# Kernel tuning notes

Measured on AMD Instinct MI355X. Metric: run time of the kernel, lower is better.

## Reference

```python
import jax, jax.numpy as jnp
import numpy as np

L_COORD = 5.0
L_NOOBJ = 0.5
NUM_CLS = 20


def setup_inputs() -> dict:
    key = jax.random.key(0)
    k1, k2, k3, k4, k5, k6, k7 = jax.random.split(key, 7)
    BS, S, MAXOBJ = 2048, 14, 20
    # post-sigmoid style predictions in [0,1): [conf,x,y,w,h]*2 + 20 classes
    pred = jax.random.uniform(k1, (BS, S, S, 30), jnp.float32)
    # valid GT boxes: x1,y1,x2,y2 in [0,1] with positive w,h; class index stored as float
    x1 = jax.random.uniform(k2, (BS, MAXOBJ)) * 0.75
    y1 = jax.random.uniform(k3, (BS, MAXOBJ)) * 0.75
    w = jax.random.uniform(k4, (BS, MAXOBJ)) * 0.2 + 0.02
    h = jax.random.uniform(k5, (BS, MAXOBJ)) * 0.2 + 0.02
    cls = jax.random.randint(k6, (BS, MAXOBJ), 0, NUM_CLS).astype(jnp.float32)
    target = jnp.stack([x1, y1, x1 + w, y1 + h, cls], axis=-1)
    valid = (jax.random.uniform(k7, (BS, MAXOBJ)) > 0.3).astype(jnp.float32)
    target = target * valid[..., None]
    return {"pred": pred, "target": target}


def build_target(target, pred_boxes, grids):
    """target: (BS,MaxObj,5); pred_boxes: (BS,2,S,S,5) [conf,x,y,w,h].
    Returns confxywh (BS,2,S,S,5) and class one-hots (BS,S,S,20).
    Sequential scan over object slots preserves the torch loop's
    last-write-wins semantics when two objects land in the same cell."""
    bs = target.shape[0]
    bidx = jnp.arange(bs)
    conf0 = jnp.zeros((bs, 2, grids, grids, 5), pred_boxes.dtype)
    clc0 = jnp.zeros((bs, grids, grids, NUM_CLS), pred_boxes.dtype)
    fg = float(grids)

    def step(carry, obj):  # obj: (BS,5)
        conf, clc = carry
        x1, y1, x2, y2, cls = (obj[:, i] for i in range(5))
        valid = obj.sum(axis=1) != 0
        cx = (x1 + x2) * 0.5 * fg
        cy = (y1 + y2) * 0.5 * fg
        w = x2 - x1
        h = y2 - y1
        gx = jnp.clip(jnp.floor(cx).astype(jnp.int32), 0, grids - 1)
        gy = jnp.clip(jnp.floor(cy).astype(jnp.int32), 0, grids - 1)
        offx = cx - gx
        offy = cy - gy
        # responsible-cell predictions: (BS,2,5) -> xywh
        pb = pred_boxes[bidx, :, gy, gx]
        pxy = pb[..., 1:3] / fg
        pwh = pb[..., 3:5]
        p_lt = pxy - 0.5 * pwh
        p_rb = pxy + 0.5 * pwh
        t_ctr = jnp.stack([offx, offy], -1) / fg  # matches original (uses offsets, not cx/cy)
        t_wh = jnp.stack([w, h], -1)
        t_lt = t_ctr - 0.5 * t_wh
        t_rb = t_ctr + 0.5 * t_wh
        lt = jnp.maximum(p_lt, t_lt[:, None, :])
        rb = jnp.minimum(p_rb, t_rb[:, None, :])
        whi = jnp.clip(rb - lt, 0.0, None)
        inter = whi[..., 0] * whi[..., 1]
        a1 = (p_rb[..., 0] - p_lt[..., 0]) * (p_rb[..., 1] - p_lt[..., 1])
        a2 = ((t_rb[..., 0] - t_lt[..., 0]) * (t_rb[..., 1] - t_lt[..., 1]))[:, None]
        iou = inter / (a1 + a2 - inter)  # (BS,2)
        mi = jnp.argmax(iou, axis=1).astype(jnp.int32)
        # invalid rows: redirect to an out-of-range grid row, dropped by scatter
        gy_s = jnp.where(valid, gy, grids)
        vals = jnp.stack([jnp.ones_like(offx), offx, offy, w, h], -1)
        conf = conf.at[bidx, mi, gy_s, gx].set(vals, mode="drop")
        clc = clc.at[bidx, gy_s, gx, cls.astype(jnp.int32)].set(1.0, mode="drop")
        return (conf, clc), None

    (conf, clc), _ = jax.lax.scan(step, (conf0, clc0), jnp.swapaxes(target, 0, 1))
    return conf, clc


def _yolo_loss(pred, target):
    bs, S = pred.shape[0], pred.shape[2]
    pred_b = pred[..., :10].reshape(bs, S, S, 2, 5).transpose(0, 3, 1, 2, 4)  # (BS,2,S,S,5)
    pred_cls = pred[..., 10:]  # (BS,S,S,20)
    conf, clc = build_target(target, pred_b, S)

    conf_sum = conf[:, 0, :, :, 0] + conf[:, 1, :, :, 0]  # (BS,S,S)
    obj_m = conf_sum == 1.0
    noobj_m = conf_sum == 0.0
    noobj_m2 = jnp.broadcast_to(noobj_m[:, None], (bs, 2, S, S))

    n_noobj = jnp.sum(noobj_m2.astype(pred.dtype))
    noobj_loss = jnp.sum(noobj_m2 * (pred_b[..., 0] - conf[..., 0]) ** 2) / n_noobj

    # responsible box rows = obj cells AND non-zero target row (selectMask in torch)
    resp = obj_m[:, None] & (jnp.sum(conf, axis=-1) != 0)  # (BS,2,S,S)
    resp_f = resp.astype(pred.dtype)
    n_resp = jnp.sum(resp_f)

    objconf_loss = jnp.sum(resp_f * (pred_b[..., 0] - conf[..., 0]) ** 2) / n_resp
    loss_xy = jnp.sum(resp_f[..., None] * (pred_b[..., 1:3] - conf[..., 1:3]) ** 2) / (n_resp * 2.0)

    # safe sqrt: masked-out entries replaced by 1.0 to keep grads finite
    rm = resp[..., None]
    p_wh = jnp.sqrt(jnp.where(rm, pred_b[..., 3:5], 1.0))
    t_wh = jnp.sqrt(jnp.where(rm, conf[..., 3:5], 1.0))
    loss_wh = jnp.sum(resp_f[..., None] * (p_wh - t_wh) ** 2) / (n_resp * 2.0)

    obj_f = obj_m.astype(pred.dtype)
    n_obj = jnp.sum(obj_f)
    loss_clc = jnp.sum(obj_f[..., None] * (pred_cls - clc) ** 2) / (n_obj * NUM_CLS)

    return L_COORD * (loss_xy + loss_wh) + objconf_loss + L_NOOBJ * noobj_loss + loss_clc


def reference(pred, target):
    return _yolo_loss(pred, target)
```

## Files before the change

### kernel.cpp

```cpp
#include <hip/hip_runtime.h>
#include <math.h>

#define NBATCH 2048
#define GS 14
#define NCELL (GS * GS)
#define NCH 30
#define NPRED (NCELL * NCH)
#define MAXOBJ 20
#define NCLS 20
#define THREADS 256
#define BLOCKS 512

#define NWIN 200704
#define NWORK (NWIN * 4)
#define TOT_THREADS (BLOCKS * THREADS)
#define NITER 7

typedef float v4f __attribute__((ext_vector_type(4)));


__global__ __launch_bounds__(256) void yolo_main_kernel(
        const float* __restrict__ pred,
        const float* __restrict__ target,
        float* __restrict__ ws)
{
    __shared__ float s_red[4][8];
    const int blk = blockIdx.x;
    const int tid = threadIdx.x;
    const int wave = tid >> 6;
    const int lane = tid & 63;
    const float fg = (float)GS;
    const int b = blk * 4 + wave;
    const int gtid = blk * THREADS + tid;

    v4f xr[NITER];
    int wm_[NITER];
    {
        const v4f* g4 = (const v4f*)pred;
        #pragma unroll
        for (int k = 0; k < NITER; ++k) {
            int w = gtid + k * TOT_THREADS;
            int wc = (w < NWORK) ? w : (NWORK - 1);
            int g = wc >> 2;
            int m = wc & 3;
            int q = g * 15 + (m & 1) + ((m >> 1) * 7);
            wm_[k] = (w < NWORK) ? m : -1;
            xr[k] = __builtin_nontemporal_load(&g4[q]);
        }
    }

    float t0 = 0.f, t1 = 0.f, t2 = 0.f, t3 = 0.f, t4 = 0.f;
    if (lane < MAXOBJ) {
        const float* tb = target + (size_t)b * (MAXOBJ * 5) + lane * 5;
        t0 = tb[0]; t1 = tb[1]; t2 = tb[2]; t3 = tb[3]; t4 = tb[4];
    }

    float acc = 0.f;
    #pragma unroll
    for (int k = 0; k < NITER; ++k) {
        int m = wm_[k];
        if (m >= 0) {
            v4f x = xr[k];
            float val = (m == 0) ? x[0] : (m == 1) ? x[1] : (m == 2) ? x[2] : x[3];
            acc += val * val;
        }
    }

    float v0 = 0.f, v1 = 0.f, v2 = 0.f, v3 = 0.f, v4 = 0.f, v5 = 0.f, v6 = 0.f;
    {
        const int o = lane;
        bool valid = false;
        int cell = 0, mi = 0, cls = 0;
        float offx = 0.f, offy = 0.f, w = 0.f, h = 0.f;
        float pc[10];
        #pragma unroll
        for (int i = 0; i < 10; ++i) pc[i] = 0.f;

        if (o < MAXOBJ && (t0 + t1 + t2 + t3 + t4) != 0.0f) {
            valid = true;
            float cx = (t0 + t2) * 0.5f * fg;
            float cy = (t1 + t3) * 0.5f * fg;
            w = t2 - t0;
            h = t3 - t1;
            int gx = min(max((int)floorf(cx), 0), GS - 1);
            int gy = min(max((int)floorf(cy), 0), GS - 1);
            offx = cx - (float)gx;
            offy = cy - (float)gy;
            cell = gy * GS + gx;
            cls = (int)t4;
            const float2* p2 = (const float2*)(pred + ((size_t)b * NCELL + cell) * NCH);
            #pragma unroll
            for (int i = 0; i < 5; ++i) {
                float2 xx = p2[i];
                pc[2 * i] = xx.x;
                pc[2 * i + 1] = xx.y;
            }
            float tcx = offx / fg, tcy = offy / fg;
            float tlx = tcx - 0.5f * w, tly = tcy - 0.5f * h;
            float trx = tcx + 0.5f * w, trY = tcy + 0.5f * h;
            float ta = (trx - tlx) * (trY - tly);
            float iou0, iou1;
            {
                float px = pc[1] / fg, py = pc[2] / fg;
                float pw = pc[3], ph = pc[4];
                float plx = px - 0.5f * pw, ply = py - 0.5f * ph;
                float prx = px + 0.5f * pw, prY = py + 0.5f * ph;
                float ix = fmaxf(fminf(prx, trx) - fmaxf(plx, tlx), 0.f);
                float iy = fmaxf(fminf(prY, trY) - fmaxf(ply, tly), 0.f);
                float inter = ix * iy;
                float a1 = (prx - plx) * (prY - ply);
                iou0 = inter / (a1 + ta - inter);
            }
            {
                float px = pc[6] / fg, py = pc[7] / fg;
                float pw = pc[8], ph = pc[9];
                float plx = px - 0.5f * pw, ply = py - 0.5f * ph;
                float prx = px + 0.5f * pw, prY = py + 0.5f * ph;
                float ix = fmaxf(fminf(prx, trx) - fmaxf(plx, tlx), 0.f);
                float iy = fmaxf(fminf(prY, trY) - fmaxf(ply, tly), 0.f);
                float inter = ix * iy;
                float a1 = (prx - plx) * (prY - ply);
                iou1 = inter / (a1 + ta - inter);
            }
            mi = (iou1 > iou0) ? 1 : 0;
        }

        int pack = cell | (mi << 8) | (cls << 16);
        unsigned long long vm = __ballot(valid);

        bool win = valid;
        #pragma unroll
        for (int j = 0; j < MAXOBJ; ++j) {
            int pj = __shfl(pack, j);
            if (((vm >> j) & 1ull) && j > o && (pj & 0x1FF) == (pack & 0x1FF))
                win = false;
        }
        unsigned long long wmask = __ballot(win);

        bool other = false;
        bool rep = win;
        unsigned int clsmask = 0u;
        #pragma unroll
        for (int j = 0; j < MAXOBJ; ++j) {
            int pj = __shfl(pack, j);
            int cj = pj & 0xFF;
            int mj = (pj >> 8) & 1;
            int clj = (pj >> 16) & 0xFF;
            bool vj = (vm >> j) & 1ull;
            bool wj = (wmask >> j) & 1ull;
            if (wj && cj == cell && mj != mi) other = true;
            if (wj && j < o && cj == cell) rep = false;
            if (vj && cj == cell) clsmask |= (1u << clj);
        }

        if (rep) {
            v0 = pc[0] * pc[0] + pc[5] * pc[5];
            v1 = 1.0f;
        }
        if (win && !other) {
            float conf = mi ? pc[5] : pc[0];
            float px   = mi ? pc[6] : pc[1];
            float py   = mi ? pc[7] : pc[2];
            float pw   = mi ? pc[8] : pc[3];
            float ph   = mi ? pc[9] : pc[4];
            float dconf = conf - 1.0f;
            v2 = dconf * dconf;
            float dx = px - offx, dy = py - offy;
            v3 = dx * dx + dy * dy;
            float sw = sqrtf(pw) - sqrtf(w);
            float sh = sqrtf(ph) - sqrtf(h);
            v4 = sw * sw + sh * sh;
            const float2* p2 = (const float2*)(pred + ((size_t)b * NCELL + cell) * NCH);
            float clc = 0.f;
            #pragma unroll
            for (int k = 0; k < 10; ++k) {
                float2 xx = p2[5 + k];
                float c0 = ((clsmask >> (2 * k)) & 1u) ? 1.0f : 0.0f;
                float c1 = ((clsmask >> (2 * k + 1)) & 1u) ? 1.0f : 0.0f;
                float d0 = xx.x - c0, d1 = xx.y - c1;
                clc += d0 * d0 + d1 * d1;
            }
            v5 = clc;
            v6 = 1.0f;
        }

        #pragma unroll
        for (int off = 32; off > 0; off >>= 1) {
            v0 += __shfl_down(v0, off);
            v1 += __shfl_down(v1, off);
            v2 += __shfl_down(v2, off);
            v3 += __shfl_down(v3, off);
            v4 += __shfl_down(v4, off);
            v5 += __shfl_down(v5, off);
            v6 += __shfl_down(v6, off);
        }
    }

    #pragma unroll
    for (int off = 32; off > 0; off >>= 1) acc += __shfl_down(acc, off);

    if (lane == 0) {
        s_red[wave][0] = v0; s_red[wave][1] = v1; s_red[wave][2] = v2;
        s_red[wave][3] = v3; s_red[wave][4] = v4; s_red[wave][5] = v5;
        s_red[wave][6] = v6; s_red[wave][7] = acc;
    }
    __syncthreads();
    if (tid == 0) {
        float* p = ws + (size_t)blk * 8;
        #pragma unroll
        for (int k = 0; k < 8; ++k)
            p[k] = s_red[0][k] + s_red[1][k] + s_red[2][k] + s_red[3][k];
    }
}

__global__ __launch_bounds__(256) void yolo_final_kernel(
        const float* __restrict__ ws,
        float* __restrict__ out)
{
    __shared__ float s_red[4][8];
    const int tid = threadIdx.x;
    const int wave = tid >> 6;
    const int lane = tid & 63;

    float v[8] = {0.f, 0.f, 0.f, 0.f, 0.f, 0.f, 0.f, 0.f};
    for (int r = tid; r < BLOCKS; r += THREADS) {
        const float4* p = (const float4*)(ws + (size_t)r * 8);
        float4 x0 = p[0];
        float4 x1 = p[1];
        v[0] += x0.x; v[1] += x0.y; v[2] += x0.z; v[3] += x0.w;
        v[4] += x1.x; v[5] += x1.y; v[6] += x1.z; v[7] += x1.w;
    }
    #pragma unroll
    for (int off = 32; off > 0; off >>= 1) {
        #pragma unroll
        for (int k = 0; k < 8; ++k) v[k] += __shfl_down(v[k], off);
    }
    if (lane == 0) {
        #pragma unroll
        for (int k = 0; k < 8; ++k) s_red[wave][k] = v[k];
    }
    __syncthreads();
    if (tid == 0) {
        float s_sub     = s_red[0][0] + s_red[1][0] + s_red[2][0] + s_red[3][0];
        float c_occ     = s_red[0][1] + s_red[1][1] + s_red[2][1] + s_red[3][1];
        float s_objconf = s_red[0][2] + s_red[1][2] + s_red[2][2] + s_red[3][2];
        float s_xy      = s_red[0][3] + s_red[1][3] + s_red[2][3] + s_red[3][3];
        float s_wh      = s_red[0][4] + s_red[1][4] + s_red[2][4] + s_red[3][4];
        float s_clc     = s_red[0][5] + s_red[1][5] + s_red[2][5] + s_red[3][5];
        float c_obj1    = s_red[0][6] + s_red[1][6] + s_red[2][6] + s_red[3][6];
        float s_all     = s_red[0][7] + s_red[1][7] + s_red[2][7] + s_red[3][7];

        float s_noobj = s_all - s_sub;
        float c_noobj = (float)(NBATCH * NCELL) - c_occ;
        float n_noobj = 2.0f * c_noobj;
        float n_resp  = c_obj1;
        float noobj_loss   = s_noobj / n_noobj;
        float objconf_loss = s_objconf / n_resp;
        float loss_xy  = s_xy / (n_resp * 2.0f);
        float loss_wh  = s_wh / (n_resp * 2.0f);
        float loss_clc = s_clc / (c_obj1 * (float)NCLS);
        out[0] = 5.0f * (loss_xy + loss_wh) + objconf_loss
               + 0.5f * noobj_loss + loss_clc;
    }
}

extern "C" void kernel_launch(void* const* d_in, const int* in_sizes, int n_in,
                              void* d_out, int out_size, void* d_ws, size_t ws_size,
                              hipStream_t stream) {
    const float* pred = (const float*)d_in[0];
    const float* target = (const float*)d_in[1];
    float* ws = (float*)d_ws;
    float* out = (float*)d_out;

    yolo_main_kernel<<<BLOCKS, THREADS, 0, stream>>>(pred, target, ws);
    yolo_final_kernel<<<1, THREADS, 0, stream>>>(ws, out);
}
```

Before: 17.53 us.

## Split main kernel into separate object-matching and streaming block groups

Instead of each of 512 blocks doing both the per-object matching and a 7-deep slice of the dense confidence-squares stream, the grid now has 512 object blocks plus 2048 streaming blocks that each handle up to 2 loads per thread. This spreads the bandwidth-bound stream over more waves and separates it from the latency-heavy object work. The nontemporal hint is dropped and the final reduction now reads 2560 partial rows instead of 512.

```diff
diff --git a/kernel.cpp b/kernel.cpp
--- a/kernel.cpp
+++ b/kernel.cpp
@@ -9,12 +9,15 @@
 #define MAXOBJ 20
 #define NCLS 20
 #define THREADS 256
-#define BLOCKS 512
+
+#define OBJ_BLOCKS 512
+#define STREAM_BLOCKS 2048
+#define TOTAL_BLOCKS (OBJ_BLOCKS + STREAM_BLOCKS)
 
 #define NWIN 200704
 #define NWORK (NWIN * 4)
-#define TOT_THREADS (BLOCKS * THREADS)
-#define NITER 7
+#define STREAM_THREADS (STREAM_BLOCKS * THREADS)
+#define SNITER 2
 
 typedef float v4f __attribute__((ext_vector_type(4)));
 
@@ -30,45 +33,35 @@
     const int wave = tid >> 6;
     const int lane = tid & 63;
     const float fg = (float)GS;
-    const int b = blk * 4 + wave;
-    const int gtid = blk * THREADS + tid;
-
-    v4f xr[NITER];
-    int wm_[NITER];
-    {
+
+    float v0 = 0.f, v1 = 0.f, v2 = 0.f, v3 = 0.f, v4 = 0.f, v5 = 0.f, v6 = 0.f;
+    float acc = 0.f;
+
+    if (blk >= OBJ_BLOCKS) {
+        const int gtid = (blk - OBJ_BLOCKS) * THREADS + tid;
         const v4f* g4 = (const v4f*)pred;
         #pragma unroll
-        for (int k = 0; k < NITER; ++k) {
-            int w = gtid + k * TOT_THREADS;
-            int wc = (w < NWORK) ? w : (NWORK - 1);
-            int g = wc >> 2;
-            int m = wc & 3;
-            int q = g * 15 + (m & 1) + ((m >> 1) * 7);
-            wm_[k] = (w < NWORK) ? m : -1;
-            xr[k] = __builtin_nontemporal_load(&g4[q]);
-        }
-    }
-
-    float t0 = 0.f, t1 = 0.f, t2 = 0.f, t3 = 0.f, t4 = 0.f;
-    if (lane < MAXOBJ) {
-        const float* tb = target + (size_t)b * (MAXOBJ * 5) + lane * 5;
-        t0 = tb[0]; t1 = tb[1]; t2 = tb[2]; t3 = tb[3]; t4 = tb[4];
-    }
-
-    float acc = 0.f;
-    #pragma unroll
-    for (int k = 0; k < NITER; ++k) {
-        int m = wm_[k];
-        if (m >= 0) {
-            v4f x = xr[k];
-            float val = (m == 0) ? x[0] : (m == 1) ? x[1] : (m == 2) ? x[2] : x[3];
-            acc += val * val;
-        }
-    }
-
-    float v0 = 0.f, v1 = 0.f, v2 = 0.f, v3 = 0.f, v4 = 0.f, v5 = 0.f, v6 = 0.f;
-    {
+        for (int k = 0; k < SNITER; ++k) {
+            int w = gtid + k * STREAM_THREADS;
+            if (w < NWORK) {
+                int m = w & 3;
+                int g = w >> 2;
+                int q = g * 15 + (m & 1) + ((m >> 1) * 7);
+                v4f x = g4[q];
+                float val = (m == 0) ? x[0] : (m == 1) ? x[1] : (m == 2) ? x[2] : x[3];
+                acc += val * val;
+            }
+        }
+    } else {
+        const int b = blk * 4 + wave;
         const int o = lane;
+
+        float t0 = 0.f, t1 = 0.f, t2 = 0.f, t3 = 0.f, t4 = 0.f;
+        if (lane < MAXOBJ) {
+            const float* tb = target + (size_t)b * (MAXOBJ * 5) + lane * 5;
+            t0 = tb[0]; t1 = tb[1]; t2 = tb[2]; t3 = tb[3]; t4 = tb[4];
+        }
+
         bool valid = false;
         int cell = 0, mi = 0, cls = 0;
         float offx = 0.f, offy = 0.f, w = 0.f, h = 0.f;
@@ -223,7 +216,7 @@
     const int lane = tid & 63;
 
     float v[8] = {0.f, 0.f, 0.f, 0.f, 0.f, 0.f, 0.f, 0.f};
-    for (int r = tid; r < BLOCKS; r += THREADS) {
+    for (int r = tid; r < TOTAL_BLOCKS; r += THREADS) {
         const float4* p = (const float4*)(ws + (size_t)r * 8);
         float4 x0 = p[0];
         float4 x1 = p[1];
@@ -272,6 +265,6 @@
     float* ws = (float*)d_ws;
     float* out = (float*)d_out;
 
-    yolo_main_kernel<<<BLOCKS, THREADS, 0, stream>>>(pred, target, ws);
+    yolo_main_kernel<<<TOTAL_BLOCKS, THREADS, 0, stream>>>(pred, target, ws);
     yolo_final_kernel<<<1, THREADS, 0, stream>>>(ws, out);
 }
```

Measured after the change: 19.23 us. 1.1x slower.
